# Optimization experiments

Hardware: AMD Instinct MI355X
Metric: run time of the kernel (lower is better)

Reference implementation:

```python
import jax, jax.numpy as jnp
import numpy as np

B, S, H = 16, 2048, 1024

def setup_inputs() -> dict:
    key = jax.random.key(0)
    ks = jax.random.split(key, 6)
    return {
        "h": jax.random.normal(ks[0], (1, B, H), jnp.float32),
        "c": jax.random.normal(ks[1], (1, B, H), jnp.float32),
        "encoder_outputs": jax.random.normal(ks[2], (B, S, H), jnp.float32),
        "attn_W": jax.random.normal(ks[3], (H, 2 * H), jnp.float32) * 0.02,
        "attn_b": jax.random.normal(ks[4], (H,), jnp.float32) * 0.02,
        "v_W": jax.random.normal(ks[5], (1, H), jnp.float32) * 0.02,
    }

def reference(h, c, encoder_outputs, attn_W, attn_b, v_W):
    # h: (1,B,H) -> (B,1,H); a: (B,S,H)
    a = encoder_outputs
    hq = jnp.transpose(h, (1, 0, 2))  # (B,1,H)
    # cat((s, a), -1) @ attn_W.T == s @ Wh.T + a @ Wa.T (avoids (B,S,2H) buffer)
    Wh, Wa = attn_W[:, :H], attn_W[:, H:]
    energy = jax.nn.relu(
        jnp.einsum("bqh,oh->bqo", hq, Wh)          # (B,1,H), broadcast over S
        + jnp.einsum("bsh,oh->bso", a, Wa)
        + attn_b
    )  # (B,S,H)
    scores = jnp.einsum("bsh,h->bs", energy, v_W[0])  # (B,S)
    attn_weights = jax.nn.softmax(scores, axis=1)      # (B,S)
    context = jnp.einsum("bs,bsh->bh", attn_weights, a)[:, None, :]  # (B,1,H)
    return context, attn_weights
```

## Files before the change

kernel.cpp:

```cpp
#include <hip/hip_runtime.h>
#include <hip/hip_bf16.h>


typedef __bf16 bf16x8 __attribute__((ext_vector_type(8)));
typedef float floatx4 __attribute__((ext_vector_type(4)));

#define BB 16
#define SS 2048
#define HH 1024
#define MM (BB * SS)

#define GLB(p) ((const __attribute__((address_space(1))) void*)(p))
#define LDSP(p) ((__attribute__((address_space(3))) void*)(p))

__device__ inline ushort f2bf(float x) {
    uint32_t u = __builtin_bit_cast(uint32_t, x);
    u += 0x7FFFu + ((u >> 16) & 1u);
    return (ushort)(u >> 16);
}

__global__ __launch_bounds__(256) void convert_A_kernel(
    const float* __restrict__ src, __bf16* __restrict__ dst)
{
    size_t i = (size_t)blockIdx.x * 256 + threadIdx.x;
    const float* s = src + i * 8;
    float4 a = *(const float4*)(s);
    float4 b = *(const float4*)(s + 4);
    union { ushort u[8]; uint4 v; } p;
    p.u[0] = f2bf(a.x); p.u[1] = f2bf(a.y); p.u[2] = f2bf(a.z); p.u[3] = f2bf(a.w);
    p.u[4] = f2bf(b.x); p.u[5] = f2bf(b.y); p.u[6] = f2bf(b.z); p.u[7] = f2bf(b.w);
    *(uint4*)(dst + i * 8) = p.v;
}

__global__ __launch_bounds__(256) void convert_W_kernel(
    const float* __restrict__ W, __bf16* __restrict__ Wb)
{
    int i = blockIdx.x * 256 + threadIdx.x;
    int o = i >> 7;
    int k = (i & 127) * 8;
    const float* s = W + (size_t)o * (2 * HH) + HH + k;
    float4 a = *(const float4*)(s);
    float4 b = *(const float4*)(s + 4);
    union { ushort u[8]; uint4 v; } p;
    p.u[0] = f2bf(a.x); p.u[1] = f2bf(a.y); p.u[2] = f2bf(a.z); p.u[3] = f2bf(a.w);
    p.u[4] = f2bf(b.x); p.u[5] = f2bf(b.y); p.u[6] = f2bf(b.z); p.u[7] = f2bf(b.w);
    *(uint4*)(Wb + (size_t)o * HH + k) = p.v;
}

__global__ __launch_bounds__(256) void projh_kernel(
    const float* __restrict__ h, const float* __restrict__ W,
    const float* __restrict__ bias, float* __restrict__ projh)
{
    int b = blockIdx.x >> 4;
    int oc = blockIdx.x & 15;
    int tid = threadIdx.x;
    __shared__ float hrow[HH];
    *(float4*)&hrow[tid * 4] = *(const float4*)(h + (size_t)b * HH + tid * 4);
    __syncthreads();
    int ol = tid >> 2;
    int kq = tid & 3;
    int o = oc * 64 + ol;
    const float* wr = W + (size_t)o * (2 * HH) + kq * 256;
    const float* hb = hrow + kq * 256;
    float sum = 0.f;
    for (int k = 0; k < 256; k += 4) {
        float4 wv = *(const float4*)(wr + k);
        sum += hb[k] * wv.x + hb[k + 1] * wv.y + hb[k + 2] * wv.z + hb[k + 3] * wv.w;
    }
    sum += __shfl_xor(sum, 1);
    sum += __shfl_xor(sum, 2);
    if (kq == 0) projh[b * HH + o] = sum + bias[o];
}

__global__ __launch_bounds__(256) void gemm_scores_kernel(
    const __bf16* __restrict__ Ab,
    const __bf16* __restrict__ Wb,
    const float* __restrict__ projh,
    const float* __restrict__ vW,
    float* __restrict__ scores)
{
    constexpr int BM = 128, BN = 128, BK = 32;

    __shared__ __bf16 As[BM * BK];
    __shared__ __bf16 Bs[BN * BK];

    const int n0 = blockIdx.x * BN;
    const int m0 = blockIdx.y * BM;
    const int bidx = m0 >> 11;

    const int tid = threadIdx.x;
    const int lane = tid & 63;
    const int wave = tid >> 6;
    const int wm = (wave & 1) * 64;
    const int wn = (wave >> 1) * 64;
    const int quad = lane >> 4;
    const int l16 = lane & 15;

    floatx4 acc[4][4];
    const floatx4 z = {0.f, 0.f, 0.f, 0.f};
#pragma unroll
    for (int i = 0; i < 4; i++)
#pragma unroll
        for (int j = 0; j < 4; j++) acc[i][j] = z;

    int g_row[4], g_col[4];
#pragma unroll
    for (int is = 0; is < 4; is++) {
        int part = is & 1;
        int c = part * 256 + tid;
        int u = c >> 3, j = c & 7;
        int jj = j ^ (u & 7);
        g_row[is] = u * 2 + (jj >> 2);
        g_col[is] = (jj & 3) * 8;
    }
    const __bf16* gA0 = Ab + (size_t)(m0 + g_row[0]) * HH + g_col[0];
    const __bf16* gA1 = Ab + (size_t)(m0 + g_row[1]) * HH + g_col[1];
    const __bf16* gB0 = Wb + (size_t)(n0 + g_row[2]) * HH + g_col[2];
    const __bf16* gB1 = Wb + (size_t)(n0 + g_row[3]) * HH + g_col[3];
    __bf16* lA0 = As + (size_t)wave * 512;
    __bf16* lA1 = As + 2048 + (size_t)wave * 512;
    __bf16* lB0 = Bs + (size_t)wave * 512;
    __bf16* lB1 = Bs + 2048 + (size_t)wave * 512;

    const __bf16* aaddr[4];
    const __bf16* baddr[4];
#pragma unroll
    for (int i = 0; i < 4; i++) {
        int frow = wm + i * 16 + l16;
        int u = frow >> 1;
        int cc = u * 8 + (((((frow & 1) << 2) | quad)) ^ (u & 7));
        aaddr[i] = &As[cc * 8];
        frow = wn + i * 16 + l16;
        u = frow >> 1;
        cc = u * 8 + (((((frow & 1) << 2) | quad)) ^ (u & 7));
        baddr[i] = &Bs[cc * 8];
    }

    for (int k0 = 0; k0 < HH; k0 += BK) {
        __syncthreads();
        __builtin_amdgcn_global_load_lds(GLB(gA0 + k0), LDSP(lA0), 16, 0, 0);
        __builtin_amdgcn_global_load_lds(GLB(gA1 + k0), LDSP(lA1), 16, 0, 0);
        __builtin_amdgcn_global_load_lds(GLB(gB0 + k0), LDSP(lB0), 16, 0, 0);
        __builtin_amdgcn_global_load_lds(GLB(gB1 + k0), LDSP(lB1), 16, 0, 0);
        __syncthreads();

        bf16x8 af[4], bf[4];
#pragma unroll
        for (int i = 0; i < 4; i++) af[i] = *(const bf16x8*)aaddr[i];
#pragma unroll
        for (int j = 0; j < 4; j++) bf[j] = *(const bf16x8*)baddr[j];
#pragma unroll
        for (int i = 0; i < 4; i++)
#pragma unroll
            for (int j = 0; j < 4; j++)
                acc[i][j] = __builtin_amdgcn_mfma_f32_16x16x32_bf16(af[i], bf[j], acc[i][j], 0, 0, 0);
    }

    float ph[4], vv[4];
#pragma unroll
    for (int j = 0; j < 4; j++) {
        int ng = n0 + wn + j * 16 + l16;
        ph[j] = projh[bidx * HH + ng];
        vv[j] = vW[ng];
    }
#pragma unroll
    for (int i = 0; i < 4; i++) {
        float s[4] = {0.f, 0.f, 0.f, 0.f};
#pragma unroll
        for (int j = 0; j < 4; j++) {
#pragma unroll
            for (int r = 0; r < 4; r++) {
                float e = acc[i][j][r] + ph[j];
                e = e > 0.f ? e : 0.f;
                s[r] += e * vv[j];
            }
        }
#pragma unroll
        for (int r = 0; r < 4; r++) {
            s[r] += __shfl_xor(s[r], 1);
            s[r] += __shfl_xor(s[r], 2);
            s[r] += __shfl_xor(s[r], 4);
            s[r] += __shfl_xor(s[r], 8);
        }
        if (l16 == 0) {
#pragma unroll
            for (int r = 0; r < 4; r++) {
                int mg = m0 + wm + i * 16 + quad * 4 + r;
                atomicAdd(&scores[mg], s[r]);
            }
        }
    }
}

__global__ __launch_bounds__(256) void gemm_scores_f32_kernel(
    const float* __restrict__ A, const float* __restrict__ W,
    const float* __restrict__ projh, const float* __restrict__ vW,
    float* __restrict__ scores)
{
    constexpr int BM = 128, BN = 128, BK = 32, LDT = BK + 8;
    __shared__ __bf16 As[BM * LDT];
    __shared__ __bf16 Bs[BN * LDT];
    const int n0 = blockIdx.x * BN;
    const int m0 = blockIdx.y * BM;
    const int bidx = m0 >> 11;
    const int tid = threadIdx.x;
    const int lane = tid & 63;
    const int wave = tid >> 6;
    const int wm = (wave & 1) * 64;
    const int wn = (wave >> 1) * 64;
    const int quad = lane >> 4;
    const int l16 = lane & 15;
    floatx4 acc[4][4];
    const floatx4 z = {0.f, 0.f, 0.f, 0.f};
#pragma unroll
    for (int i = 0; i < 4; i++)
#pragma unroll
        for (int j = 0; j < 4; j++) acc[i][j] = z;
    int rowT[4], colT[4];
#pragma unroll
    for (int i = 0; i < 4; i++) {
        int fi = tid + 256 * i;
        rowT[i] = fi >> 3;
        colT[i] = (fi & 7) * 4;
    }
    for (int k0 = 0; k0 < HH; k0 += BK) {
        float4 av[4], bv[4];
#pragma unroll
        for (int i = 0; i < 4; i++) {
            av[i] = *(const float4*)(A + (size_t)(m0 + rowT[i]) * HH + k0 + colT[i]);
            bv[i] = *(const float4*)(W + (size_t)(n0 + rowT[i]) * (2 * HH) + HH + k0 + colT[i]);
        }
        __syncthreads();
#pragma unroll
        for (int i = 0; i < 4; i++) {
            ushort4 ua = make_ushort4(f2bf(av[i].x), f2bf(av[i].y), f2bf(av[i].z), f2bf(av[i].w));
            ushort4 ub = make_ushort4(f2bf(bv[i].x), f2bf(bv[i].y), f2bf(bv[i].z), f2bf(bv[i].w));
            *(ushort4*)&As[rowT[i] * LDT + colT[i]] = ua;
            *(ushort4*)&Bs[rowT[i] * LDT + colT[i]] = ub;
        }
        __syncthreads();
        bf16x8 af[4], bf[4];
#pragma unroll
        for (int i = 0; i < 4; i++)
            af[i] = *(const bf16x8*)&As[(wm + i * 16 + l16) * LDT + quad * 8];
#pragma unroll
        for (int j = 0; j < 4; j++)
            bf[j] = *(const bf16x8*)&Bs[(wn + j * 16 + l16) * LDT + quad * 8];
#pragma unroll
        for (int i = 0; i < 4; i++)
#pragma unroll
            for (int j = 0; j < 4; j++)
                acc[i][j] = __builtin_amdgcn_mfma_f32_16x16x32_bf16(af[i], bf[j], acc[i][j], 0, 0, 0);
    }
    float ph[4], vv[4];
#pragma unroll
    for (int j = 0; j < 4; j++) {
        int ng = n0 + wn + j * 16 + l16;
        ph[j] = projh[bidx * HH + ng];
        vv[j] = vW[ng];
    }
#pragma unroll
    for (int i = 0; i < 4; i++) {
        float s[4] = {0.f, 0.f, 0.f, 0.f};
#pragma unroll
        for (int j = 0; j < 4; j++) {
#pragma unroll
            for (int r = 0; r < 4; r++) {
                float e = acc[i][j][r] + ph[j];
                e = e > 0.f ? e : 0.f;
                s[r] += e * vv[j];
            }
        }
#pragma unroll
        for (int r = 0; r < 4; r++) {
            s[r] += __shfl_xor(s[r], 1);
            s[r] += __shfl_xor(s[r], 2);
            s[r] += __shfl_xor(s[r], 4);
            s[r] += __shfl_xor(s[r], 8);
        }
        if (l16 == 0) {
#pragma unroll
            for (int r = 0; r < 4; r++) {
                int mg = m0 + wm + i * 16 + quad * 4 + r;
                atomicAdd(&scores[mg], s[r]);
            }
        }
    }
}

__global__ __launch_bounds__(256) void softmax_kernel(
    const float* __restrict__ scores, float* __restrict__ wout)
{
    int b = blockIdx.x;
    int tid = threadIdx.x;
    const float* row = scores + b * SS;
    float x[8];
    float mx = -1e30f;
#pragma unroll
    for (int i = 0; i < 8; i++) { x[i] = row[tid + i * 256]; mx = fmaxf(mx, x[i]); }
#pragma unroll
    for (int off = 32; off; off >>= 1) mx = fmaxf(mx, __shfl_xor(mx, off));
    __shared__ float redm[4], reds[4];
    if ((tid & 63) == 0) redm[tid >> 6] = mx;
    __syncthreads();
    mx = fmaxf(fmaxf(redm[0], redm[1]), fmaxf(redm[2], redm[3]));
    float sum = 0.f;
#pragma unroll
    for (int i = 0; i < 8; i++) { x[i] = __expf(x[i] - mx); sum += x[i]; }
#pragma unroll
    for (int off = 32; off; off >>= 1) sum += __shfl_xor(sum, off);
    if ((tid & 63) == 0) reds[tid >> 6] = sum;
    __syncthreads();
    float inv = 1.0f / (reds[0] + reds[1] + reds[2] + reds[3]);
#pragma unroll
    for (int i = 0; i < 8; i++) wout[b * SS + tid + i * 256] = x[i] * inv;
}

__global__ __launch_bounds__(256) void context_kernel(
    const float* __restrict__ A, const float* __restrict__ wgt, float* __restrict__ ctx)
{
    int b = blockIdx.x >> 4;
    int sc = blockIdx.x & 15;
    int tid = threadIdx.x;
    const float* arow = A + ((size_t)b * SS + sc * 128) * HH + tid * 4;
    const float* wrow = wgt + b * SS + sc * 128;
    float4 acc = make_float4(0.f, 0.f, 0.f, 0.f);
#pragma unroll 4
    for (int s = 0; s < 128; s++) {
        float w = wrow[s];
        float4 v = *(const float4*)(arow + (size_t)s * HH);
        acc.x += w * v.x; acc.y += w * v.y; acc.z += w * v.z; acc.w += w * v.w;
    }
    float* o = ctx + b * HH + tid * 4;
    atomicAdd(o + 0, acc.x);
    atomicAdd(o + 1, acc.y);
    atomicAdd(o + 2, acc.z);
    atomicAdd(o + 3, acc.w);
}

extern "C" void kernel_launch(void* const* d_in, const int* in_sizes, int n_in,
                              void* d_out, int out_size, void* d_ws, size_t ws_size,
                              hipStream_t stream) {
    const float* h    = (const float*)d_in[0];
    const float* a    = (const float*)d_in[2];
    const float* W    = (const float*)d_in[3];
    const float* bias = (const float*)d_in[4];
    const float* vW   = (const float*)d_in[5];
    float* out = (float*)d_out;

    float* projh  = (float*)d_ws;
    float* scores = projh + BB * HH;
    __bf16* Wb = (__bf16*)(scores + MM);
    __bf16* Ab = Wb + (size_t)HH * HH;
    const size_t need = (size_t)(BB * HH + MM) * 4 + (size_t)HH * HH * 2
                      + (size_t)MM * HH * 2;

    hipMemsetAsync(scores, 0, (size_t)MM * sizeof(float), stream);
    hipMemsetAsync(out, 0, (size_t)BB * HH * sizeof(float), stream);

    projh_kernel<<<BB * 16, 256, 0, stream>>>(h, W, bias, projh);

    if (ws_size >= need) {
        convert_A_kernel<<<(MM * HH / 8) / 256, 256, 0, stream>>>(a, Ab);
        convert_W_kernel<<<(HH * HH / 8) / 256, 256, 0, stream>>>(W, Wb);
        gemm_scores_kernel<<<dim3(HH / 128, MM / 128), 256, 0, stream>>>(Ab, Wb, projh, vW, scores);
    } else {
        gemm_scores_f32_kernel<<<dim3(HH / 128, MM / 128), 256, 0, stream>>>(a, W, projh, vW, scores);
    }

    softmax_kernel<<<BB, 256, 0, stream>>>(scores, out + BB * HH);
    context_kernel<<<BB * 16, 256, 0, stream>>>(a, out + BB * HH, out);
}
```

Measured before the change: 340.7 us.

## Merge prep launches and memsets into one kernel; group-swizzle GEMM block order

Folds the projh computation, the W-to-bf16 conversion and the zeroing of scores and context into a single prep kernel selected by block-index ranges. This replaces two memsets and two kernel launches with one launch. It also switches the scores GEMM to a 1D grid with grouped tile ordering: 8 M-tiles by 8 N-tiles per group of 64 blocks, meant to improve L2 reuse of A and W tiles. In the fallback path prep also writes Wb, which that path never uses.

```diff
diff --git a/kernel.cpp b/kernel.cpp
--- a/kernel.cpp
+++ b/kernel.cpp
@@ -32,44 +32,55 @@
     *(uint4*)(dst + i * 8) = p.v;
 }
 
-__global__ __launch_bounds__(256) void convert_W_kernel(
-    const float* __restrict__ W, __bf16* __restrict__ Wb)
-{
-    int i = blockIdx.x * 256 + threadIdx.x;
-    int o = i >> 7;
-    int k = (i & 127) * 8;
-    const float* s = W + (size_t)o * (2 * HH) + HH + k;
-    float4 a = *(const float4*)(s);
-    float4 b = *(const float4*)(s + 4);
-    union { ushort u[8]; uint4 v; } p;
-    p.u[0] = f2bf(a.x); p.u[1] = f2bf(a.y); p.u[2] = f2bf(a.z); p.u[3] = f2bf(a.w);
-    p.u[4] = f2bf(b.x); p.u[5] = f2bf(b.y); p.u[6] = f2bf(b.z); p.u[7] = f2bf(b.w);
-    *(uint4*)(Wb + (size_t)o * HH + k) = p.v;
-}
-
-__global__ __launch_bounds__(256) void projh_kernel(
+__global__ __launch_bounds__(256) void prep_kernel(
     const float* __restrict__ h, const float* __restrict__ W,
-    const float* __restrict__ bias, float* __restrict__ projh)
-{
-    int b = blockIdx.x >> 4;
-    int oc = blockIdx.x & 15;
+    const float* __restrict__ bias, float* __restrict__ projh,
+    __bf16* __restrict__ Wb, float* __restrict__ scores, float* __restrict__ ctx)
+{
+    int bid = blockIdx.x;
     int tid = threadIdx.x;
-    __shared__ float hrow[HH];
-    *(float4*)&hrow[tid * 4] = *(const float4*)(h + (size_t)b * HH + tid * 4);
-    __syncthreads();
-    int ol = tid >> 2;
-    int kq = tid & 3;
-    int o = oc * 64 + ol;
-    const float* wr = W + (size_t)o * (2 * HH) + kq * 256;
-    const float* hb = hrow + kq * 256;
-    float sum = 0.f;
-    for (int k = 0; k < 256; k += 4) {
-        float4 wv = *(const float4*)(wr + k);
-        sum += hb[k] * wv.x + hb[k + 1] * wv.y + hb[k + 2] * wv.z + hb[k + 3] * wv.w;
-    }
-    sum += __shfl_xor(sum, 1);
-    sum += __shfl_xor(sum, 2);
-    if (kq == 0) projh[b * HH + o] = sum + bias[o];
+    if (bid < 256) {
+        int b = bid >> 4;
+        int oc = bid & 15;
+        __shared__ float hrow[HH];
+        *(float4*)&hrow[tid * 4] = *(const float4*)(h + (size_t)b * HH + tid * 4);
+        __syncthreads();
+        int ol = tid >> 2;
+        int kq = tid & 3;
+        int o = oc * 64 + ol;
+        const float* wr = W + (size_t)o * (2 * HH) + kq * 256;
+        const float* hb = hrow + kq * 256;
+        float sum = 0.f;
+        for (int k = 0; k < 256; k += 4) {
+            float4 wv = *(const float4*)(wr + k);
+            sum += hb[k] * wv.x + hb[k + 1] * wv.y + hb[k + 2] * wv.z + hb[k + 3] * wv.w;
+        }
+        sum += __shfl_xor(sum, 1);
+        sum += __shfl_xor(sum, 2);
+        if (kq == 0) projh[b * HH + o] = sum + bias[o];
+    } else if (bid < 320) {
+        int cb = bid - 256;
+#pragma unroll
+        for (int j = 0; j < 8; j++) {
+            int g = cb * 2048 + tid + j * 256;
+            int o = g >> 7;
+            int k = (g & 127) * 8;
+            const float* s = W + (size_t)o * (2 * HH) + HH + k;
+            float4 a = *(const float4*)(s);
+            float4 b2 = *(const float4*)(s + 4);
+            union { ushort u[8]; uint4 v; } p;
+            p.u[0] = f2bf(a.x); p.u[1] = f2bf(a.y); p.u[2] = f2bf(a.z); p.u[3] = f2bf(a.w);
+            p.u[4] = f2bf(b2.x); p.u[5] = f2bf(b2.y); p.u[6] = f2bf(b2.z); p.u[7] = f2bf(b2.w);
+            *(uint4*)(Wb + (size_t)o * HH + k) = p.v;
+        }
+    } else {
+        int zb = bid - 320;
+        float4 z = make_float4(0.f, 0.f, 0.f, 0.f);
+        float* sp = scores + zb * 2048 + tid * 8;
+        *(float4*)(sp) = z;
+        *(float4*)(sp + 4) = z;
+        *(float4*)(ctx + zb * 1024 + tid * 4) = z;
+    }
 }
 
 __global__ __launch_bounds__(256) void gemm_scores_kernel(
@@ -84,8 +95,12 @@
     __shared__ __bf16 As[BM * BK];
     __shared__ __bf16 Bs[BN * BK];
 
-    const int n0 = blockIdx.x * BN;
-    const int m0 = blockIdx.y * BM;
+    const int bid = blockIdx.x;
+    const int grp = bid >> 6;
+    const int r   = bid & 63;
+    const int n0 = (r >> 3) * BN;
+    const int my = grp * 8 + (r & 7);
+    const int m0 = my * BM;
     const int bidx = m0 >> 11;
 
     const int tid = threadIdx.x;
@@ -169,24 +184,24 @@
 #pragma unroll
         for (int j = 0; j < 4; j++) {
 #pragma unroll
-            for (int r = 0; r < 4; r++) {
-                float e = acc[i][j][r] + ph[j];
+            for (int r2 = 0; r2 < 4; r2++) {
+                float e = acc[i][j][r2] + ph[j];
                 e = e > 0.f ? e : 0.f;
-                s[r] += e * vv[j];
+                s[r2] += e * vv[j];
             }
         }
 #pragma unroll
-        for (int r = 0; r < 4; r++) {
-            s[r] += __shfl_xor(s[r], 1);
-            s[r] += __shfl_xor(s[r], 2);
-            s[r] += __shfl_xor(s[r], 4);
-            s[r] += __shfl_xor(s[r], 8);
+        for (int r2 = 0; r2 < 4; r2++) {
+            s[r2] += __shfl_xor(s[r2], 1);
+            s[r2] += __shfl_xor(s[r2], 2);
+            s[r2] += __shfl_xor(s[r2], 4);
+            s[r2] += __shfl_xor(s[r2], 8);
         }
         if (l16 == 0) {
 #pragma unroll
-            for (int r = 0; r < 4; r++) {
-                int mg = m0 + wm + i * 16 + quad * 4 + r;
-                atomicAdd(&scores[mg], s[r]);
+            for (int r2 = 0; r2 < 4; r2++) {
+                int mg = m0 + wm + i * 16 + quad * 4 + r2;
+                atomicAdd(&scores[mg], s[r2]);
             }
         }
     }
@@ -355,16 +370,12 @@
     const size_t need = (size_t)(BB * HH + MM) * 4 + (size_t)HH * HH * 2
                       + (size_t)MM * HH * 2;
 
-    hipMemsetAsync(scores, 0, (size_t)MM * sizeof(float), stream);
-    hipMemsetAsync(out, 0, (size_t)BB * HH * sizeof(float), stream);
-
-    projh_kernel<<<BB * 16, 256, 0, stream>>>(h, W, bias, projh);
-
     if (ws_size >= need) {
+        prep_kernel<<<336, 256, 0, stream>>>(h, W, bias, projh, Wb, scores, out);
         convert_A_kernel<<<(MM * HH / 8) / 256, 256, 0, stream>>>(a, Ab);
-        convert_W_kernel<<<(HH * HH / 8) / 256, 256, 0, stream>>>(W, Wb);
-        gemm_scores_kernel<<<dim3(HH / 128, MM / 128), 256, 0, stream>>>(Ab, Wb, projh, vW, scores);
+        gemm_scores_kernel<<<2048, 256, 0, stream>>>(Ab, Wb, projh, vW, scores);
     } else {
+        prep_kernel<<<336, 256, 0, stream>>>(h, W, bias, projh, Wb, scores, out);
         gemm_scores_f32_kernel<<<dim3(HH / 128, MM / 128), 256, 0, stream>>>(a, W, projh, vW, scores);
     }
 
```

After: 323.7 us. 5.0% less time.
